# Kernel tuning notes

Measured on AMD Instinct MI355X. Metric: run time of the kernel, lower is better.

Reference implementation:

```python
import jax, jax.numpy as jnp
import numpy as np

N = 524288          # batch size
NUM_SD = 64         # socio-demographic chars
H = 128             # hidden size of TasteParams MLP
NUM_ALT_FEAT = 9    # alternative features
NUM_CLASSES = 3
# utility_structure: class k -> (start, end) column slice of x
SEGMENTS = [(0, 3), (3, 6), (6, 9)]


def setup_inputs() -> dict:
    key = jax.random.key(0)
    ks = jax.random.split(key, 8)
    s = 0.05
    return {
        "x": jax.random.normal(ks[0], (N, NUM_ALT_FEAT), jnp.float32),
        "z": jax.random.normal(ks[1], (N, NUM_SD), jnp.float32),
        "W1": jax.random.normal(ks[2], (NUM_SD, H), jnp.float32) * s,
        "b1": jax.random.normal(ks[3], (H,), jnp.float32) * s,
        "W2": jax.random.normal(ks[4], (H, H), jnp.float32) * s,
        "b2": jax.random.normal(ks[5], (H,), jnp.float32) * s,
        "W3": jax.random.normal(ks[6], (H, NUM_ALT_FEAT + NUM_CLASSES), jnp.float32) * s,
        "b3": jax.random.normal(ks[7], (NUM_ALT_FEAT + NUM_CLASSES,), jnp.float32) * s,
    }


def _forward(x, z, W1, b1, W2, b2, W3, b3):
    # TasteParams MLP: Linear-ReLU-Linear-ReLU-Linear
    h = jax.nn.relu(z @ W1 + b1)
    h = jax.nn.relu(h @ W2 + b2)
    b = h @ W3 + b3                        # (N, 12)
    # monotonic_constraints (num_classes==3, func_intercept=True)
    b = jnp.concatenate([
        -jax.nn.relu(-b[:, :6]),
        b[:, 6:7],
        -jax.nn.relu(-b[:, 7:9]),
        b[:, -NUM_CLASSES:],
    ], axis=1)
    taste = b[:, :NUM_ALT_FEAT]            # (N, 9)
    intercept = b[:, -NUM_CLASSES:]        # (N, 3)
    # MNL_layer with b: per-segment elementwise mult + reduce into logits column
    prod = x * taste                       # (N, 9)
    logits = jnp.stack(
        [prod[:, lo:hi].sum(axis=1) for (lo, hi) in SEGMENTS], axis=1
    )                                      # (N, 3)
    return logits + intercept


def reference(x, z, W1, b1, W2, b2, W3, b3):
    return _forward(x, z, W1, b1, W2, b2, W3, b3)
```

## Files before the change

kernel.cpp:

```cpp
#include <hip/hip_runtime.h>
#include <hip/hip_bf16.h>


typedef __bf16 bf16x8 __attribute__((ext_vector_type(8)));
typedef float  f32x16 __attribute__((ext_vector_type(16)));
typedef unsigned int uint2v __attribute__((ext_vector_type(2)));
typedef unsigned int uint4v __attribute__((ext_vector_type(4)));

#define MFMA32(a, b, c) __builtin_amdgcn_mfma_f32_32x32x16_bf16((a), (b), (c), 0, 0, 0)

#define SW3 0
#define SW1 1536
#define SW2 9728
#define SB1 26112
#define SB2 26240
#define SB3 26368
#define SMEM_ELTS 26384

#define NBLK    512
#define NTILE   16384
#define WSTRIDE (NBLK * 4)

__device__ __forceinline__ unsigned pkbf(float lo, float hi) {
  unsigned short lb = __builtin_bit_cast(unsigned short, (__bf16)lo);
  unsigned short hb = __builtin_bit_cast(unsigned short, (__bf16)hi);
  return ((unsigned)hb << 16) | (unsigned)lb;
}

template <int SUB>
__device__ __forceinline__ bf16x8 mk_bfrag(const f32x16 h) {
  constexpr int B = SUB * 8;
  unsigned p01 = pkbf(h[B + 0], h[B + 1]);
  unsigned p23 = pkbf(h[B + 2], h[B + 3]);
  unsigned p45 = pkbf(h[B + 4], h[B + 5]);
  unsigned p67 = pkbf(h[B + 6], h[B + 7]);
  unsigned d0, d1, d2, d3;
#if __has_builtin(__builtin_amdgcn_permlane32_swap)
  uint2v r1 = __builtin_amdgcn_permlane32_swap(p01, p45, false, false);
  uint2v r2 = __builtin_amdgcn_permlane32_swap(p23, p67, false, false);
  d0 = r1[0]; d2 = r1[1];
  d1 = r2[0]; d3 = r2[1];
#else
  int hi = (threadIdx.x >> 5) & 1;
  unsigned sp01 = (unsigned)__shfl_xor((int)p01, 32, 64);
  unsigned sp23 = (unsigned)__shfl_xor((int)p23, 32, 64);
  unsigned sp45 = (unsigned)__shfl_xor((int)p45, 32, 64);
  unsigned sp67 = (unsigned)__shfl_xor((int)p67, 32, 64);
  d0 = hi ? sp45 : p01;
  d2 = hi ? p45  : sp01;
  d1 = hi ? sp67 : p23;
  d3 = hi ? p67  : sp23;
#endif
  uint4v t; t[0] = d0; t[1] = d1; t[2] = d2; t[3] = d3;
  return __builtin_bit_cast(bf16x8, t);
}

__device__ __forceinline__ bf16x8 ldw(const __bf16* sm, int byteoff) {
  return *(const bf16x8*)((const char*)sm + byteoff);
}

__device__ __forceinline__ bf16x8 biasA(__bf16 v) {
  bf16x8 f;
  #pragma unroll
  for (int i = 0; i < 8; ++i) f[i] = (__bf16)0.0f;
  f[0] = v;
  return f;
}

__global__ __launch_bounds__(256, 1)
void tastenet_kernel(const float* __restrict__ x, const float* __restrict__ z,
                     const float* __restrict__ W1, const float* __restrict__ b1,
                     const float* __restrict__ W2, const float* __restrict__ b2,
                     const float* __restrict__ W3, const float* __restrict__ b3,
                     float* __restrict__ out) {
  __shared__ __align__(16) __bf16 sm[SMEM_ELTS];
  const int tid = threadIdx.x;
  unsigned* smw = (unsigned*)sm;

  for (int i = tid; i < 4096; i += 256) {
    int m = i & 127, k = (i >> 7) * 2;
    smw[SW1 / 2 + m * 32 + (((k >> 3) ^ (m & 7)) << 2) + ((k >> 1) & 3)] =
        pkbf(W1[k * 128 + m], W1[(k + 1) * 128 + m]);
  }
  for (int i = tid; i < 8192; i += 256) {
    int m = i & 127, k = (i >> 7) * 2;
    smw[SW2 / 2 + m * 64 + (((k >> 3) ^ (m & 7)) << 2) + ((k >> 1) & 3)] =
        pkbf(W2[k * 128 + m], W2[(k + 1) * 128 + m]);
  }
  for (int i = tid; i < 768; i += 256) {
    int kk = i / 12, m = i - kk * 12, k = kk * 2;
    smw[SW3 / 2 + m * 64 + (((k >> 3) ^ (m & 7)) << 2) + ((k >> 1) & 3)] =
        pkbf(W3[k * 12 + m], W3[(k + 1) * 12 + m]);
  }
  if (tid < 128) { sm[SB1 + tid] = (__bf16)b1[tid]; sm[SB2 + tid] = (__bf16)b2[tid]; }
  if (tid < 12)  sm[SB3 + tid] = (__bf16)b3[tid];
  __syncthreads();

  const int wave = tid >> 6;
  const int lane = tid & 63;
  const int q    = lane >> 5;
  const int n    = lane & 31;
  const int s8   = n & 7;
  const int eq   = q ^ (s8 & 1);
  const int sh   = s8 >> 1;

  int t1k[4], t2k[8];
  #pragma unroll
  for (int kt = 0; kt < 4; ++kt) t1k[kt] = n * 128 + eq * 16 + 32 * (kt ^ sh);
  #pragma unroll
  for (int kt = 0; kt < 8; ++kt)
    t2k[kt] = n * 256 + eq * 16 + 32 * ((kt & 3) ^ sh) + 128 * (kt >> 2);

  __bf16 bv1[4], bv2[4], bv3;
  #pragma unroll
  for (int f = 0; f < 4; ++f) {
    bv1[f] = (q == 0) ? sm[SB1 + f * 32 + n] : (__bf16)0.0f;
    bv2[f] = (q == 0) ? sm[SB2 + f * 32 + n] : (__bf16)0.0f;
  }
  bv3 = (q == 0 && n < 12) ? sm[SB3 + n] : (__bf16)0.0f;

  bf16x8 ones;
  #pragma unroll
  for (int i = 0; i < 8; ++i) ones[i] = (__bf16)0.0f;
  if (q == 0) ones[0] = (__bf16)1.0f;

  const int wid = blockIdx.x * 4 + wave;

  float4 zv[8];
  {
    const float* zr = z + ((long)wid * 32 + n) * 64;
    #pragma unroll
    for (int kt = 0; kt < 4; ++kt) {
      zv[2 * kt]     = *(const float4*)(zr + kt * 16 + q * 8);
      zv[2 * kt + 1] = *(const float4*)(zr + kt * 16 + q * 8 + 4);
    }
  }

  for (int t = wid; t < NTILE; t += WSTRIDE) {
    const long row = (long)t * 32 + n;

    const float* xr = x + row * 9;
    float xv0 = xr[q * 4 + 0], xv1 = xr[q * 4 + 1];
    float xv2 = xr[q * 4 + 2], xv3 = xr[q * 4 + 3];
    float xv4 = xr[8];

    bf16x8 bz[4];
    #pragma unroll
    for (int kt = 0; kt < 4; ++kt) {
      float4 a = zv[2 * kt], b = zv[2 * kt + 1];
      bf16x8 f;
      f[0] = (__bf16)a.x; f[1] = (__bf16)a.y; f[2] = (__bf16)a.z; f[3] = (__bf16)a.w;
      f[4] = (__bf16)b.x; f[5] = (__bf16)b.y; f[6] = (__bf16)b.z; f[7] = (__bf16)b.w;
      bz[kt] = f;
    }

    bf16x8 bf2[8];
    #pragma unroll
    for (int fp = 0; fp < 2; ++fp) {
      f32x16 aA, aB;
      #pragma unroll
      for (int i = 0; i < 16; ++i) { aA[i] = 0.0f; aB[i] = 0.0f; }
      #pragma unroll
      for (int kt = 0; kt < 4; ++kt) {
        aA = MFMA32(ldw(sm, SW1 * 2 + (2 * fp + 0) * 4096 + t1k[kt]), bz[kt], aA);
        aB = MFMA32(ldw(sm, SW1 * 2 + (2 * fp + 1) * 4096 + t1k[kt]), bz[kt], aB);
      }
      aA = MFMA32(biasA(bv1[2 * fp + 0]), ones, aA);
      aB = MFMA32(biasA(bv1[2 * fp + 1]), ones, aB);
      #pragma unroll
      for (int i = 0; i < 16; ++i) { aA[i] = fmaxf(aA[i], 0.0f); aB[i] = fmaxf(aB[i], 0.0f); }
      bf2[4 * fp + 0] = mk_bfrag<0>(aA);
      bf2[4 * fp + 1] = mk_bfrag<1>(aA);
      bf2[4 * fp + 2] = mk_bfrag<0>(aB);
      bf2[4 * fp + 3] = mk_bfrag<1>(aB);
    }

    bf16x8 bf3[8];
    #pragma unroll
    for (int fp = 0; fp < 2; ++fp) {
      f32x16 aA, aB;
      #pragma unroll
      for (int i = 0; i < 16; ++i) { aA[i] = 0.0f; aB[i] = 0.0f; }
      #pragma unroll
      for (int kt = 0; kt < 8; ++kt) {
        aA = MFMA32(ldw(sm, SW2 * 2 + (2 * fp + 0) * 8192 + t2k[kt]), bf2[kt], aA);
        aB = MFMA32(ldw(sm, SW2 * 2 + (2 * fp + 1) * 8192 + t2k[kt]), bf2[kt], aB);
      }
      aA = MFMA32(biasA(bv2[2 * fp + 0]), ones, aA);
      aB = MFMA32(biasA(bv2[2 * fp + 1]), ones, aB);
      #pragma unroll
      for (int i = 0; i < 16; ++i) { aA[i] = fmaxf(aA[i], 0.0f); aB[i] = fmaxf(aB[i], 0.0f); }
      bf3[4 * fp + 0] = mk_bfrag<0>(aA);
      bf3[4 * fp + 1] = mk_bfrag<1>(aA);
      bf3[4 * fp + 2] = mk_bfrag<0>(aB);
      bf3[4 * fp + 3] = mk_bfrag<1>(aB);
    }

    if (t + WSTRIDE < NTILE) {
      const float* zr = z + ((long)(t + WSTRIDE) * 32 + n) * 64;
      #pragma unroll
      for (int kt = 0; kt < 4; ++kt) {
        zv[2 * kt]     = *(const float4*)(zr + kt * 16 + q * 8);
        zv[2 * kt + 1] = *(const float4*)(zr + kt * 16 + q * 8 + 4);
      }
    }

    f32x16 acc3;
    #pragma unroll
    for (int i = 0; i < 16; ++i) acc3[i] = 0.0f;
    #pragma unroll
    for (int kt = 0; kt < 8; ++kt)
      acc3 = MFMA32(ldw(sm, SW3 * 2 + t2k[kt]), bf3[kt], acc3);
    acc3 = MFMA32(biasA(bv3), ones, acc3);

    float t0 = acc3[0], t1 = acc3[1], t2 = acc3[2], t3 = acc3[3];
    float t4 = acc3[4], t5 = acc3[5], t6 = acc3[6], t7 = acc3[7];
    float o0 = 0.f, o1 = 0.f, o2 = 0.f, g1v = 0.f, g2v = 0.f;
    if (q == 0) {
      t0 = fminf(t0, 0.0f); t1 = fminf(t1, 0.0f);
      t2 = fminf(t2, 0.0f); t3 = fminf(t3, 0.0f);
      t4 = fminf(t4, 0.0f);
      o0 = xv0 * t0 + xv1 * t1 + xv2 * t2 + t5;
      o1 = xv3 * t3 + t6;
      o2 = xv4 * t4 + t7;
    } else {
      t0 = fminf(t0, 0.0f); t1 = fminf(t1, 0.0f);
      t3 = fminf(t3, 0.0f);
      g1v = xv0 * t0 + xv1 * t1;
      g2v = xv2 * t2 + xv3 * t3;
    }
    float a1v = __shfl_xor(g1v, 32, 64);
    float a2v = __shfl_xor(g2v, 32, 64);
    if (q == 0) {
      float* op = out + row * 3;
      op[0] = o0;
      op[1] = o1 + a1v;
      op[2] = o2 + a2v;
    }
  }
}

extern "C" void kernel_launch(void* const* d_in, const int* in_sizes, int n_in,
                              void* d_out, int out_size, void* d_ws, size_t ws_size,
                              hipStream_t stream) {
  const float* x  = (const float*)d_in[0];
  const float* z  = (const float*)d_in[1];
  const float* W1 = (const float*)d_in[2];
  const float* b1 = (const float*)d_in[3];
  const float* W2 = (const float*)d_in[4];
  const float* b2 = (const float*)d_in[5];
  const float* W3 = (const float*)d_in[6];
  const float* b3 = (const float*)d_in[7];
  tastenet_kernel<<<dim3(NBLK), dim3(256), 0, stream>>>(
      x, z, W1, b1, W2, b2, W3, b3, (float*)d_out);
}
```

Before: 250.6 us.

## Double-buffer z prefetch two tiles ahead and split layer-3 MFMA chain

Keeps two register buffers of z rows and issues the global load for the tile two iterations ahead right after converting the current one, so the load has a whole tile of compute to hide behind. The loop is manually unrolled by two with a lambda body. The layer-3 MFMA chain is split into two independent accumulators that are summed afterwards, which shortens the dependency chain. This costs extra VGPRs for the second z buffer and accumulator, which may add pressure or cause spills.

```diff
diff --git a/kernel.cpp b/kernel.cpp
--- a/kernel.cpp
+++ b/kernel.cpp
@@ -126,17 +126,23 @@
 
   const int wid = blockIdx.x * 4 + wave;
 
-  float4 zv[8];
+  float4 zvA[8], zvB[8];
   {
     const float* zr = z + ((long)wid * 32 + n) * 64;
     #pragma unroll
     for (int kt = 0; kt < 4; ++kt) {
-      zv[2 * kt]     = *(const float4*)(zr + kt * 16 + q * 8);
-      zv[2 * kt + 1] = *(const float4*)(zr + kt * 16 + q * 8 + 4);
-    }
-  }
-
-  for (int t = wid; t < NTILE; t += WSTRIDE) {
+      zvA[2 * kt]     = *(const float4*)(zr + kt * 16 + q * 8);
+      zvA[2 * kt + 1] = *(const float4*)(zr + kt * 16 + q * 8 + 4);
+    }
+    const float* zr2 = z + ((long)(wid + WSTRIDE) * 32 + n) * 64;
+    #pragma unroll
+    for (int kt = 0; kt < 4; ++kt) {
+      zvB[2 * kt]     = *(const float4*)(zr2 + kt * 16 + q * 8);
+      zvB[2 * kt + 1] = *(const float4*)(zr2 + kt * 16 + q * 8 + 4);
+    }
+  }
+
+  auto body = [&](int t, float4* zv) {
     const long row = (long)t * 32 + n;
 
     const float* xr = x + row * 9;
@@ -152,6 +158,15 @@
       f[0] = (__bf16)a.x; f[1] = (__bf16)a.y; f[2] = (__bf16)a.z; f[3] = (__bf16)a.w;
       f[4] = (__bf16)b.x; f[5] = (__bf16)b.y; f[6] = (__bf16)b.z; f[7] = (__bf16)b.w;
       bz[kt] = f;
+    }
+
+    if (t + 2 * WSTRIDE < NTILE) {
+      const float* zr = z + ((long)(t + 2 * WSTRIDE) * 32 + n) * 64;
+      #pragma unroll
+      for (int kt = 0; kt < 4; ++kt) {
+        zv[2 * kt]     = *(const float4*)(zr + kt * 16 + q * 8);
+        zv[2 * kt + 1] = *(const float4*)(zr + kt * 16 + q * 8 + 4);
+      }
     }
 
     bf16x8 bf2[8];
@@ -196,25 +211,20 @@
       bf3[4 * fp + 3] = mk_bfrag<1>(aB);
     }
 
-    if (t + WSTRIDE < NTILE) {
-      const float* zr = z + ((long)(t + WSTRIDE) * 32 + n) * 64;
-      #pragma unroll
-      for (int kt = 0; kt < 4; ++kt) {
-        zv[2 * kt]     = *(const float4*)(zr + kt * 16 + q * 8);
-        zv[2 * kt + 1] = *(const float4*)(zr + kt * 16 + q * 8 + 4);
-      }
-    }
-
-    f32x16 acc3;
-    #pragma unroll
-    for (int i = 0; i < 16; ++i) acc3[i] = 0.0f;
-    #pragma unroll
-    for (int kt = 0; kt < 8; ++kt)
-      acc3 = MFMA32(ldw(sm, SW3 * 2 + t2k[kt]), bf3[kt], acc3);
-    acc3 = MFMA32(biasA(bv3), ones, acc3);
-
-    float t0 = acc3[0], t1 = acc3[1], t2 = acc3[2], t3 = acc3[3];
-    float t4 = acc3[4], t5 = acc3[5], t6 = acc3[6], t7 = acc3[7];
+    f32x16 a3a, a3b;
+    #pragma unroll
+    for (int i = 0; i < 16; ++i) { a3a[i] = 0.0f; a3b[i] = 0.0f; }
+    #pragma unroll
+    for (int kt = 0; kt < 4; ++kt) {
+      a3a = MFMA32(ldw(sm, SW3 * 2 + t2k[kt]), bf3[kt], a3a);
+      a3b = MFMA32(ldw(sm, SW3 * 2 + t2k[kt + 4]), bf3[kt + 4], a3b);
+    }
+    a3a = MFMA32(biasA(bv3), ones, a3a);
+
+    float t0 = a3a[0] + a3b[0], t1 = a3a[1] + a3b[1];
+    float t2 = a3a[2] + a3b[2], t3 = a3a[3] + a3b[3];
+    float t4 = a3a[4] + a3b[4], t5 = a3a[5] + a3b[5];
+    float t6 = a3a[6] + a3b[6], t7 = a3a[7] + a3b[7];
     float o0 = 0.f, o1 = 0.f, o2 = 0.f, g1v = 0.f, g2v = 0.f;
     if (q == 0) {
       t0 = fminf(t0, 0.0f); t1 = fminf(t1, 0.0f);
@@ -237,6 +247,12 @@
       op[1] = o1 + a1v;
       op[2] = o2 + a2v;
     }
+  };
+
+  #pragma unroll 1
+  for (int t = wid; t < NTILE; t += 2 * WSTRIDE) {
+    body(t, zvA);
+    body(t + WSTRIDE, zvB);
   }
 }
 
```

New measurement: 278.4 us. 11.1% more time.
